# Kernel tuning notes

Measured on AMD Instinct MI355X. Metric: run time of the kernel, lower is better.

The kernel has to match this reference:

```python
import jax, jax.numpy as jnp
import numpy as np

B, S, D = 16, 2048, 128


def setup_inputs() -> dict:
    k = jax.random.key(0)
    k1, k2, k3, k4 = jax.random.split(k, 4)
    query = jax.random.normal(k1, (B, S, D), dtype=jnp.float32)
    key = jax.random.normal(k2, (B, S, D), dtype=jnp.float32)
    value = jax.random.normal(k3, (B, S, D), dtype=jnp.float32)
    # per-query tensor-valued inverse scale; shift away from zero for stable division
    inv_scale_factor = jax.random.uniform(k4, (B, S, 1), dtype=jnp.float32) + 0.5
    dropout_p = jnp.float32(0.1)
    return {"query": query, "key": key, "value": value,
            "inv_scale_factor": inv_scale_factor, "dropout_p": dropout_p}


def reference(query, key, value, inv_scale_factor, dropout_p):
    # QK^T: [B, Sq, Sk]
    qk = jnp.einsum('bqd,bkd->bqk', query, key)
    # tensor-valued scale divide (broadcast [B, Sq, 1] over keys)
    scaled_qk = qk / inv_scale_factor
    softmax_qk = jax.nn.softmax(scaled_qk, axis=-1)
    # dropout with a fixed RNG key (deterministic reference)
    keep_prob = 1.0 - dropout_p
    mask = jax.random.bernoulli(jax.random.key(42), keep_prob, softmax_qk.shape)
    dropout_qk = jnp.where(mask, softmax_qk / keep_prob, jnp.float32(0.0))
    # AV: [B, Sq, Dv]
    return jnp.einsum('bqk,bkv->bqv', dropout_qk, value)
```

## Files before the change

kernel.cpp:

```cpp
#include <hip/hip_runtime.h>
#include <stdint.h>


#define B_ 16
#define S_ 2048
#define D_ 128
#define TQ 64
#define TK 64
#define KSTR 136
#define VSTR 72
#define PSTR 40

typedef float f32x4 __attribute__((ext_vector_type(4)));
typedef _Float16 f16x8 __attribute__((ext_vector_type(8)));
typedef _Float16 f16x2 __attribute__((ext_vector_type(2)));

#define DPP_ROR(x, ctrl) \
  __int_as_float(__builtin_amdgcn_update_dpp(0, __float_as_int(x), (ctrl), 0xf, 0xf, true))
__device__ __forceinline__ float row16_max(float x) {
  x = fmaxf(x, DPP_ROR(x, 0x128));
  x = fmaxf(x, DPP_ROR(x, 0x124));
  x = fmaxf(x, DPP_ROR(x, 0x122));
  x = fmaxf(x, DPP_ROR(x, 0x121));
  return x;
}
__device__ __forceinline__ float row16_sum(float x) {
  x += DPP_ROR(x, 0x128);
  x += DPP_ROR(x, 0x124);
  x += DPP_ROR(x, 0x122);
  x += DPP_ROR(x, 0x121);
  return x;
}

__device__ __forceinline__ uint2 threefry2x32_0_42(uint32_t x0, uint32_t x1) {
  const uint32_t k0 = 0u, k1 = 42u;
  const uint32_t k2 = 0x1BD11BDAu ^ k0 ^ k1;
  x0 += k0; x1 += k1;
#define TFR(r) { x0 += x1; x1 = __builtin_rotateleft32(x1, r); x1 ^= x0; }
  TFR(13) TFR(15) TFR(26) TFR(6)
  x0 += k1; x1 += k2 + 1u;
  TFR(17) TFR(29) TFR(16) TFR(24)
  x0 += k2; x1 += k0 + 2u;
  TFR(13) TFR(15) TFR(26) TFR(6)
  x0 += k0; x1 += k1 + 3u;
  TFR(17) TFR(29) TFR(16) TFR(24)
  x0 += k1; x1 += k2 + 4u;
  TFR(13) TFR(15) TFR(26) TFR(6)
  x0 += k2; x1 += k0 + 5u;
#undef TFR
  return make_uint2(x0, x1);
}

__device__ __forceinline__ uint32_t jax_bits(uint32_t j) {
  const uint2 tf = threefry2x32_0_42(0u, j);
  return tf.x ^ tf.y;
}

__global__ __launch_bounds__(512, 4)
void attn_mfma_kernel(const float* __restrict__ Q, const float* __restrict__ K,
                      const float* __restrict__ V, const float* __restrict__ ISF,
                      const float* __restrict__ DP, float* __restrict__ OUT) {
  __shared__ __align__(16) char smem[46080];
  _Float16* const sK  = (_Float16*)smem;
  _Float16* const sVT = (_Float16*)(smem + 17408);
  _Float16* const sP  = (_Float16*)(smem + 35840);
  float* const sO1 = (float*)smem;
  float* const sM1 = (float*)(smem + 32768);
  float* const sL1 = (float*)(smem + 33024);

  const int t    = threadIdx.x;
  const int lane = t & 63;
  const int l15  = lane & 15;
  const int quad = lane >> 4;
  const int w    = t >> 6;
  const int qg   = w & 3;
  const int kph  = w >> 2;
  const int b    = blockIdx.y;
  const int qw   = blockIdx.x * TQ + qg * 16;

  const float kp = 1.0f - DP[0];
  const uint32_t TH9 = (__float_as_uint(1.0f + kp) & 0x7FFFFFu) << 9;

  float m_[4], l_[4];
  uint32_t jq[4];
  #pragma unroll
  for (int r = 0; r < 4; ++r) {
    m_[r] = -INFINITY;
    l_[r] = 0.0f;
    jq[r] = ((uint32_t)b << 22) + (uint32_t)(qw + quad * 4 + r) * (uint32_t)S_;
  }

  f16x8 qf[4];
  {
    const float qs = 1.4426950408889634f / ISF[b * S_ + qw + l15];
    const float* qp = Q + ((size_t)(b * S_ + qw + l15)) * D_;
    #pragma unroll
    for (int c = 0; c < 4; ++c) {
      const float4 a = *(const float4*)(qp + c * 32 + quad * 8);
      const float4 d2 = *(const float4*)(qp + c * 32 + quad * 8 + 4);
      const float xs[8] = {a.x, a.y, a.z, a.w, d2.x, d2.y, d2.z, d2.w};
      f16x8 h;
      #pragma unroll
      for (int j = 0; j < 8; ++j) h[j] = (_Float16)(xs[j] * qs);
      qf[c] = h;
    }
  }

  f32x4 accO[8];
  #pragma unroll
  for (int i = 0; i < 8; ++i) accO[i] = (f32x4){0.f, 0.f, 0.f, 0.f};

  _Float16* const pwv = &sP[w * 16 * PSTR];

  const int krow = t >> 3, kcol = (t & 7) * 16;
  const int vp = t & 31, dseg = (t >> 5) * 8;

  for (int kt = 0; kt < S_ / TK; ++kt) {
    __syncthreads();

    {
      const float* gk = K + ((size_t)(b * S_ + kt * TK + krow)) * D_ + kcol;
      float kf[16];
      #pragma unroll
      for (int i = 0; i < 4; ++i) *(float4*)&kf[i * 4] = *(const float4*)(gk + i * 4);
      #pragma unroll
      for (int g = 0; g < 2; ++g) {
        f16x8 h;
        #pragma unroll
        for (int j = 0; j < 8; ++j) h[j] = (_Float16)kf[g * 8 + j];
        *(f16x8*)&sK[krow * KSTR + kcol + g * 8] = h;
      }
    }
    {
      const float* gv = V + ((size_t)(b * S_ + kt * TK + 2 * vp)) * D_ + dseg;
      float v0[8], v1[8];
      #pragma unroll
      for (int i = 0; i < 2; ++i) {
        *(float4*)&v0[i * 4] = *(const float4*)(gv + i * 4);
        *(float4*)&v1[i * 4] = *(const float4*)(gv + D_ + i * 4);
      }
      #pragma unroll
      for (int d = 0; d < 8; ++d) {
        f16x2 h = {(_Float16)v0[d], (_Float16)v1[d]};
        *(f16x2*)&sVT[(dseg + d) * VSTR + 2 * vp] = h;
      }
    }
    __syncthreads();

    f32x4 s[2];
    #pragma unroll
    for (int n = 0; n < 2; ++n) {
      f32x4 acc = (f32x4){0.f, 0.f, 0.f, 0.f};
      #pragma unroll
      for (int c = 0; c < 4; ++c) {
        const f16x8 bh = *(const f16x8*)&sK[(kph * 32 + n * 16 + l15) * KSTR + c * 32 + quad * 8];
        acc = __builtin_amdgcn_mfma_f32_16x16x32_f16(qf[c], bh, acc, 0, 0, 0);
      }
      s[n] = acc;
    }

    float mx[4];
    #pragma unroll
    for (int r = 0; r < 4; ++r) mx[r] = row16_max(fmaxf(s[0][r], s[1][r]));
    int changed = 0;
    #pragma unroll
    for (int r = 0; r < 4; ++r) changed |= (mx[r] > m_[r]);
    if (__ballot(changed) != 0ull) {
      #pragma unroll
      for (int r = 0; r < 4; ++r) {
        const float mnew = fmaxf(m_[r], mx[r]);
        const float alpha = __builtin_amdgcn_exp2f(m_[r] - mnew);
        m_[r] = mnew;
        l_[r] *= alpha;
        #pragma unroll
        for (int i = 0; i < 8; ++i) accO[i][r] *= alpha;
      }
    }
    #pragma unroll
    for (int r = 0; r < 4; ++r) {
      const float p0 = __builtin_amdgcn_exp2f(s[0][r] - m_[r]);
      const float p1 = __builtin_amdgcn_exp2f(s[1][r] - m_[r]);
      s[0][r] = p0; s[1][r] = p1;
      l_[r] += row16_sum(p0 + p1);
    }

    #pragma unroll
    for (int n = 0; n < 2; ++n) {
      const int col = n * 16 + l15;
      const uint32_t jcol = (uint32_t)(kt * TK + kph * 32 + col);
      #pragma unroll
      for (int r = 0; r < 4; ++r) {
        const uint32_t bits = jax_bits(jq[r] + jcol);
        const float pf = (bits < TH9) ? s[n][r] : 0.0f;
        pwv[(quad * 4 + r) * PSTR + col] = (_Float16)pf;
      }
    }
    __threadfence_block();

    {
      const f16x8 ap = *(const f16x8*)&pwv[l15 * PSTR + quad * 8];
      #pragma unroll
      for (int d8 = 0; d8 < 8; ++d8) {
        const f16x8 bv = *(const f16x8*)&sVT[(d8 * 16 + l15) * VSTR + kph * 32 + quad * 8];
        accO[d8] = __builtin_amdgcn_mfma_f32_16x16x32_f16(ap, bv, accO[d8], 0, 0, 0);
      }
    }
  }

  __syncthreads();
  if (kph == 1) {
    if (l15 == 0) {
      #pragma unroll
      for (int r = 0; r < 4; ++r) {
        sM1[qg * 16 + quad * 4 + r] = m_[r];
        sL1[qg * 16 + quad * 4 + r] = l_[r];
      }
    }
    #pragma unroll
    for (int d8 = 0; d8 < 8; ++d8) {
      #pragma unroll
      for (int r = 0; r < 4; ++r)
        sO1[qg * 2048 + (quad * 4 + r) * D_ + d8 * 16 + l15] = accO[d8][r];
    }
  }
  __syncthreads();
  if (kph == 0) {
    float a0s[4], a1s[4];
    #pragma unroll
    for (int r = 0; r < 4; ++r) {
      const float m1  = sM1[qg * 16 + quad * 4 + r];
      const float l1v = sL1[qg * 16 + quad * 4 + r];
      const float mf = fmaxf(m_[r], m1);
      const float a0 = __builtin_amdgcn_exp2f(m_[r] - mf);
      const float a1 = __builtin_amdgcn_exp2f(m1 - mf);
      const float inv = 1.0f / ((a0 * l_[r] + a1 * l1v) * kp);
      a0s[r] = a0 * inv;
      a1s[r] = a1 * inv;
    }
    float* op = OUT + ((size_t)(b * S_ + qw)) * D_;
    #pragma unroll
    for (int d8 = 0; d8 < 8; ++d8) {
      #pragma unroll
      for (int r = 0; r < 4; ++r) {
        const float o1 = sO1[qg * 2048 + (quad * 4 + r) * D_ + d8 * 16 + l15];
        op[(quad * 4 + r) * D_ + d8 * 16 + l15] = accO[d8][r] * a0s[r] + o1 * a1s[r];
      }
    }
  }
}

extern "C" void kernel_launch(void* const* d_in, const int* in_sizes, int n_in,
                              void* d_out, int out_size, void* d_ws, size_t ws_size,
                              hipStream_t stream) {
  const float* q   = (const float*)d_in[0];
  const float* k   = (const float*)d_in[1];
  const float* v   = (const float*)d_in[2];
  const float* isf = (const float*)d_in[3];
  const float* dp  = (const float*)d_in[4];
  float* out = (float*)d_out;

  dim3 grid(S_ / TQ, B_);
  attn_mfma_kernel<<<grid, dim3(512), 0, stream>>>(q, k, v, isf, dp, out);
}
```

Before: 338.1 us.

## Double query tile per warp and register-prefetch next K/V tile

Each warp now handles 32 query rows (two 16-row sub-tiles) instead of 16. Each K/V tile loaded from global memory, converted to fp16 and staged in shared memory is therefore reused across twice as many queries, and the K fragments read from shared memory feed two MFMAs. The next tile's K/V global loads are issued into registers right after the barrier, so their latency overlaps the current tile's compute. The trade-off is higher register pressure (launch bounds drop to 2 blocks per CU), half as many blocks in the grid (lower occupancy), and 66.5 KB of dynamic shared memory.

```diff
diff --git a/kernel.cpp b/kernel.cpp
--- a/kernel.cpp
+++ b/kernel.cpp
@@ -5,7 +5,7 @@
 #define B_ 16
 #define S_ 2048
 #define D_ 128
-#define TQ 64
+#define TQ 128
 #define TK 64
 #define KSTR 136
 #define VSTR 72
@@ -14,6 +14,8 @@
 typedef float f32x4 __attribute__((ext_vector_type(4)));
 typedef _Float16 f16x8 __attribute__((ext_vector_type(8)));
 typedef _Float16 f16x2 __attribute__((ext_vector_type(2)));
+
+union F32R { float4 q[4]; float f[16]; };
 
 #define DPP_ROR(x, ctrl) \
   __int_as_float(__builtin_amdgcn_update_dpp(0, __float_as_int(x), (ctrl), 0xf, 0xf, true))
@@ -56,17 +58,17 @@
   return tf.x ^ tf.y;
 }
 
-__global__ __launch_bounds__(512, 4)
+__global__ __launch_bounds__(512, 2)
 void attn_mfma_kernel(const float* __restrict__ Q, const float* __restrict__ K,
                       const float* __restrict__ V, const float* __restrict__ ISF,
                       const float* __restrict__ DP, float* __restrict__ OUT) {
-  __shared__ __align__(16) char smem[46080];
+  extern __shared__ __align__(16) char smem[];
   _Float16* const sK  = (_Float16*)smem;
   _Float16* const sVT = (_Float16*)(smem + 17408);
   _Float16* const sP  = (_Float16*)(smem + 35840);
   float* const sO1 = (float*)smem;
-  float* const sM1 = (float*)(smem + 32768);
-  float* const sL1 = (float*)(smem + 33024);
+  float* const sM1 = (float*)(smem + 65536);
+  float* const sL1 = (float*)(smem + 66048);
 
   const int t    = threadIdx.x;
   const int lane = t & 63;
@@ -76,175 +78,218 @@
   const int qg   = w & 3;
   const int kph  = w >> 2;
   const int b    = blockIdx.y;
-  const int qw   = blockIdx.x * TQ + qg * 16;
+  const int qb   = blockIdx.x * TQ + qg * 32;
 
   const float kp = 1.0f - DP[0];
   const uint32_t TH9 = (__float_as_uint(1.0f + kp) & 0x7FFFFFu) << 9;
 
-  float m_[4], l_[4];
-  uint32_t jq[4];
+  float m_[2][4], l_[2][4];
+  uint32_t jq[2][4];
   #pragma unroll
-  for (int r = 0; r < 4; ++r) {
-    m_[r] = -INFINITY;
-    l_[r] = 0.0f;
-    jq[r] = ((uint32_t)b << 22) + (uint32_t)(qw + quad * 4 + r) * (uint32_t)S_;
-  }
-
-  f16x8 qf[4];
-  {
-    const float qs = 1.4426950408889634f / ISF[b * S_ + qw + l15];
-    const float* qp = Q + ((size_t)(b * S_ + qw + l15)) * D_;
+  for (int sub = 0; sub < 2; ++sub)
+    #pragma unroll
+    for (int r = 0; r < 4; ++r) {
+      m_[sub][r] = -INFINITY;
+      l_[sub][r] = 0.0f;
+      jq[sub][r] = ((uint32_t)b << 22)
+                 + (uint32_t)(qb + sub * 16 + quad * 4 + r) * (uint32_t)S_;
+    }
+
+  f16x8 qf[2][4];
+  #pragma unroll
+  for (int sub = 0; sub < 2; ++sub) {
+    const int qrow = qb + sub * 16 + l15;
+    const float qs = 1.4426950408889634f / ISF[b * S_ + qrow];
+    const float* qp = Q + ((size_t)(b * S_ + qrow)) * D_;
     #pragma unroll
     for (int c = 0; c < 4; ++c) {
-      const float4 a = *(const float4*)(qp + c * 32 + quad * 8);
+      const float4 a  = *(const float4*)(qp + c * 32 + quad * 8);
       const float4 d2 = *(const float4*)(qp + c * 32 + quad * 8 + 4);
       const float xs[8] = {a.x, a.y, a.z, a.w, d2.x, d2.y, d2.z, d2.w};
       f16x8 h;
       #pragma unroll
       for (int j = 0; j < 8; ++j) h[j] = (_Float16)(xs[j] * qs);
-      qf[c] = h;
-    }
-  }
-
-  f32x4 accO[8];
+      qf[sub][c] = h;
+    }
+  }
+
+  f32x4 accO[2][8];
   #pragma unroll
-  for (int i = 0; i < 8; ++i) accO[i] = (f32x4){0.f, 0.f, 0.f, 0.f};
-
-  _Float16* const pwv = &sP[w * 16 * PSTR];
+  for (int sub = 0; sub < 2; ++sub)
+    #pragma unroll
+    for (int i = 0; i < 8; ++i) accO[sub][i] = (f32x4){0.f, 0.f, 0.f, 0.f};
+
+  _Float16* const pwv = &sP[w * 32 * PSTR];
 
   const int krow = t >> 3, kcol = (t & 7) * 16;
   const int vp = t & 31, dseg = (t >> 5) * 8;
 
+  F32R kreg;
+  F32R vreg;
+
+#define ISSUE_LOADS(KT)                                                        \
+  {                                                                            \
+    const float4* gk4 = (const float4*)(K +                                    \
+        ((size_t)(b * S_ + (KT) * TK + krow)) * D_ + kcol);                    \
+    _Pragma("unroll") for (int i = 0; i < 4; ++i) kreg.q[i] = gk4[i];          \
+    const float4* gv4 = (const float4*)(V +                                    \
+        ((size_t)(b * S_ + (KT) * TK + 2 * vp)) * D_ + dseg);                  \
+    _Pragma("unroll") for (int i = 0; i < 2; ++i) {                            \
+      vreg.q[i] = gv4[i];                                                      \
+      vreg.q[i + 2] = gv4[i + 32];             \
+    }                                                                          \
+  }
+
+  ISSUE_LOADS(0)
+
   for (int kt = 0; kt < S_ / TK; ++kt) {
     __syncthreads();
 
     {
-      const float* gk = K + ((size_t)(b * S_ + kt * TK + krow)) * D_ + kcol;
-      float kf[16];
-      #pragma unroll
-      for (int i = 0; i < 4; ++i) *(float4*)&kf[i * 4] = *(const float4*)(gk + i * 4);
       #pragma unroll
       for (int g = 0; g < 2; ++g) {
         f16x8 h;
         #pragma unroll
-        for (int j = 0; j < 8; ++j) h[j] = (_Float16)kf[g * 8 + j];
+        for (int j = 0; j < 8; ++j) h[j] = (_Float16)kreg.f[g * 8 + j];
         *(f16x8*)&sK[krow * KSTR + kcol + g * 8] = h;
       }
     }
     {
-      const float* gv = V + ((size_t)(b * S_ + kt * TK + 2 * vp)) * D_ + dseg;
-      float v0[8], v1[8];
-      #pragma unroll
-      for (int i = 0; i < 2; ++i) {
-        *(float4*)&v0[i * 4] = *(const float4*)(gv + i * 4);
-        *(float4*)&v1[i * 4] = *(const float4*)(gv + D_ + i * 4);
-      }
       #pragma unroll
       for (int d = 0; d < 8; ++d) {
-        f16x2 h = {(_Float16)v0[d], (_Float16)v1[d]};
+        f16x2 h = {(_Float16)vreg.f[d], (_Float16)vreg.f[8 + d]};
         *(f16x2*)&sVT[(dseg + d) * VSTR + 2 * vp] = h;
       }
     }
     __syncthreads();
 
-    f32x4 s[2];
+    if (kt + 1 < S_ / TK) ISSUE_LOADS(kt + 1)
+
+    f32x4 s[2][2];
     #pragma unroll
     for (int n = 0; n < 2; ++n) {
-      f32x4 acc = (f32x4){0.f, 0.f, 0.f, 0.f};
+      f32x4 a0 = (f32x4){0.f, 0.f, 0.f, 0.f};
+      f32x4 a1 = (f32x4){0.f, 0.f, 0.f, 0.f};
       #pragma unroll
       for (int c = 0; c < 4; ++c) {
-        const f16x8 bh = *(const f16x8*)&sK[(kph * 32 + n * 16 + l15) * KSTR + c * 32 + quad * 8];
-        acc = __builtin_amdgcn_mfma_f32_16x16x32_f16(qf[c], bh, acc, 0, 0, 0);
-      }
-      s[n] = acc;
-    }
-
-    float mx[4];
-    #pragma unroll
-    for (int r = 0; r < 4; ++r) mx[r] = row16_max(fmaxf(s[0][r], s[1][r]));
+        const f16x8 bh = *(const f16x8*)&sK[(kph * 32 + n * 16 + l15) * KSTR
+                                            + c * 32 + quad * 8];
+        a0 = __builtin_amdgcn_mfma_f32_16x16x32_f16(qf[0][c], bh, a0, 0, 0, 0);
+        a1 = __builtin_amdgcn_mfma_f32_16x16x32_f16(qf[1][c], bh, a1, 0, 0, 0);
+      }
+      s[0][n] = a0;
+      s[1][n] = a1;
+    }
+
+    float mx[2][4];
     int changed = 0;
     #pragma unroll
-    for (int r = 0; r < 4; ++r) changed |= (mx[r] > m_[r]);
+    for (int sub = 0; sub < 2; ++sub)
+      #pragma unroll
+      for (int r = 0; r < 4; ++r) {
+        mx[sub][r] = row16_max(fmaxf(s[sub][0][r], s[sub][1][r]));
+        changed |= (mx[sub][r] > m_[sub][r]);
+      }
     if (__ballot(changed) != 0ull) {
       #pragma unroll
+      for (int sub = 0; sub < 2; ++sub)
+        #pragma unroll
+        for (int r = 0; r < 4; ++r) {
+          const float mnew = fmaxf(m_[sub][r], mx[sub][r]);
+          const float alpha = __builtin_amdgcn_exp2f(m_[sub][r] - mnew);
+          m_[sub][r] = mnew;
+          l_[sub][r] *= alpha;
+          #pragma unroll
+          for (int i = 0; i < 8; ++i) accO[sub][i][r] *= alpha;
+        }
+    }
+    #pragma unroll
+    for (int sub = 0; sub < 2; ++sub)
+      #pragma unroll
       for (int r = 0; r < 4; ++r) {
-        const float mnew = fmaxf(m_[r], mx[r]);
-        const float alpha = __builtin_amdgcn_exp2f(m_[r] - mnew);
-        m_[r] = mnew;
-        l_[r] *= alpha;
-        #pragma unroll
-        for (int i = 0; i < 8; ++i) accO[i][r] *= alpha;
-      }
-    }
-    #pragma unroll
-    for (int r = 0; r < 4; ++r) {
-      const float p0 = __builtin_amdgcn_exp2f(s[0][r] - m_[r]);
-      const float p1 = __builtin_amdgcn_exp2f(s[1][r] - m_[r]);
-      s[0][r] = p0; s[1][r] = p1;
-      l_[r] += row16_sum(p0 + p1);
-    }
-
-    #pragma unroll
-    for (int n = 0; n < 2; ++n) {
-      const int col = n * 16 + l15;
-      const uint32_t jcol = (uint32_t)(kt * TK + kph * 32 + col);
-      #pragma unroll
-      for (int r = 0; r < 4; ++r) {
-        const uint32_t bits = jax_bits(jq[r] + jcol);
-        const float pf = (bits < TH9) ? s[n][r] : 0.0f;
-        pwv[(quad * 4 + r) * PSTR + col] = (_Float16)pf;
-      }
-    }
+        const float p0 = __builtin_amdgcn_exp2f(s[sub][0][r] - m_[sub][r]);
+        const float p1 = __builtin_amdgcn_exp2f(s[sub][1][r] - m_[sub][r]);
+        s[sub][0][r] = p0;
+        s[sub][1][r] = p1;
+        l_[sub][r] += row16_sum(p0 + p1);
+      }
+
+    #pragma unroll
+    for (int sub = 0; sub < 2; ++sub)
+      #pragma unroll
+      for (int n = 0; n < 2; ++n) {
+        const int col = n * 16 + l15;
+        const uint32_t jcol = (uint32_t)(kt * TK + kph * 32 + col);
+        #pragma unroll
+        for (int r = 0; r < 4; ++r) {
+          const uint32_t bits = jax_bits(jq[sub][r] + jcol);
+          const float pf = (bits < TH9) ? s[sub][n][r] : 0.0f;
+          pwv[(sub * 16 + quad * 4 + r) * PSTR + col] = (_Float16)pf;
+        }
+      }
     __threadfence_block();
 
     {
-      const f16x8 ap = *(const f16x8*)&pwv[l15 * PSTR + quad * 8];
+      const f16x8 ap0 = *(const f16x8*)&pwv[l15 * PSTR + quad * 8];
+      const f16x8 ap1 = *(const f16x8*)&pwv[(16 + l15) * PSTR + quad * 8];
       #pragma unroll
       for (int d8 = 0; d8 < 8; ++d8) {
-        const f16x8 bv = *(const f16x8*)&sVT[(d8 * 16 + l15) * VSTR + kph * 32 + quad * 8];
-        accO[d8] = __builtin_amdgcn_mfma_f32_16x16x32_f16(ap, bv, accO[d8], 0, 0, 0);
-      }
-    }
-  }
+        const f16x8 bv = *(const f16x8*)&sVT[(d8 * 16 + l15) * VSTR
+                                             + kph * 32 + quad * 8];
+        accO[0][d8] = __builtin_amdgcn_mfma_f32_16x16x32_f16(ap0, bv, accO[0][d8], 0, 0, 0);
+        accO[1][d8] = __builtin_amdgcn_mfma_f32_16x16x32_f16(ap1, bv, accO[1][d8], 0, 0, 0);
+      }
+    }
+  }
+#undef ISSUE_LOADS
 
   __syncthreads();
   if (kph == 1) {
-    if (l15 == 0) {
-      #pragma unroll
-      for (int r = 0; r < 4; ++r) {
-        sM1[qg * 16 + quad * 4 + r] = m_[r];
-        sL1[qg * 16 + quad * 4 + r] = l_[r];
-      }
-    }
-    #pragma unroll
-    for (int d8 = 0; d8 < 8; ++d8) {
-      #pragma unroll
-      for (int r = 0; r < 4; ++r)
-        sO1[qg * 2048 + (quad * 4 + r) * D_ + d8 * 16 + l15] = accO[d8][r];
+    #pragma unroll
+    for (int sub = 0; sub < 2; ++sub) {
+      if (l15 == 0) {
+        #pragma unroll
+        for (int r = 0; r < 4; ++r) {
+          const int gr = qg * 32 + sub * 16 + quad * 4 + r;
+          sM1[gr] = m_[sub][r];
+          sL1[gr] = l_[sub][r];
+        }
+      }
+      #pragma unroll
+      for (int d8 = 0; d8 < 8; ++d8)
+        #pragma unroll
+        for (int r = 0; r < 4; ++r) {
+          const int gr = qg * 32 + sub * 16 + quad * 4 + r;
+          sO1[gr * D_ + d8 * 16 + l15] = accO[sub][d8][r];
+        }
     }
   }
   __syncthreads();
   if (kph == 0) {
-    float a0s[4], a1s[4];
-    #pragma unroll
-    for (int r = 0; r < 4; ++r) {
-      const float m1  = sM1[qg * 16 + quad * 4 + r];
-      const float l1v = sL1[qg * 16 + quad * 4 + r];
-      const float mf = fmaxf(m_[r], m1);
-      const float a0 = __builtin_amdgcn_exp2f(m_[r] - mf);
-      const float a1 = __builtin_amdgcn_exp2f(m1 - mf);
-      const float inv = 1.0f / ((a0 * l_[r] + a1 * l1v) * kp);
-      a0s[r] = a0 * inv;
-      a1s[r] = a1 * inv;
-    }
-    float* op = OUT + ((size_t)(b * S_ + qw)) * D_;
-    #pragma unroll
-    for (int d8 = 0; d8 < 8; ++d8) {
+    #pragma unroll
+    for (int sub = 0; sub < 2; ++sub) {
+      float a0s[4], a1s[4];
       #pragma unroll
       for (int r = 0; r < 4; ++r) {
-        const float o1 = sO1[qg * 2048 + (quad * 4 + r) * D_ + d8 * 16 + l15];
-        op[(quad * 4 + r) * D_ + d8 * 16 + l15] = accO[d8][r] * a0s[r] + o1 * a1s[r];
-      }
+        const int gr = qg * 32 + sub * 16 + quad * 4 + r;
+        const float m1  = sM1[gr];
+        const float l1v = sL1[gr];
+        const float mf = fmaxf(m_[sub][r], m1);
+        const float a0 = __builtin_amdgcn_exp2f(m_[sub][r] - mf);
+        const float a1 = __builtin_amdgcn_exp2f(m1 - mf);
+        const float inv = 1.0f / ((a0 * l_[sub][r] + a1 * l1v) * kp);
+        a0s[r] = a0 * inv;
+        a1s[r] = a1 * inv;
+      }
+      #pragma unroll
+      for (int d8 = 0; d8 < 8; ++d8)
+        #pragma unroll
+        for (int r = 0; r < 4; ++r) {
+          const int gr = qg * 32 + sub * 16 + quad * 4 + r;
+          const float o1 = sO1[gr * D_ + d8 * 16 + l15];
+          OUT[((size_t)(b * S_ + blockIdx.x * TQ + gr)) * D_ + d8 * 16 + l15] =
+              accO[sub][d8][r] * a0s[r] + o1 * a1s[r];
+        }
     }
   }
 }
@@ -260,5 +305,5 @@
   float* out = (float*)d_out;
 
   dim3 grid(S_ / TQ, B_);
-  attn_mfma_kernel<<<grid, dim3(512), 0, stream>>>(q, k, v, isf, dp, out);
-}
+  attn_mfma_kernel<<<grid, dim3(512), 66560, stream>>>(q, k, v, isf, dp, out);
+}
```

Measured after the change: 288.1 us. 1.17x faster.

## Double-buffer K/V tiles with register prefetch and double the query tile

Applied to the files above, without the earlier changes.

Doubles the query tile per block to 128 rows with 1024 threads, so each K/V tile staged in LDS is reused by twice as many query rows. The kernel now double-buffers K and V^T in LDS, using 92 KB of dynamic shared memory, and prefetches the next tile into registers while the current one is being computed. That removes one barrier per iteration and hides global-load latency. The dropout RNG bits are computed right after QK^T so the hash overlaps the softmax reductions. In exchange the grid shrinks to 256 blocks, which lowers parallelism, and the larger LDS footprint and register pressure may limit occupancy or cause spills.

```diff
diff --git a/kernel.cpp b/kernel.cpp
--- a/kernel.cpp
+++ b/kernel.cpp
@@ -5,8 +5,9 @@
 #define B_ 16
 #define S_ 2048
 #define D_ 128
-#define TQ 64
+#define TQ 128
 #define TK 64
+#define NT (S_ / TK)
 #define KSTR 136
 #define VSTR 72
 #define PSTR 40
@@ -14,6 +15,8 @@
 typedef float f32x4 __attribute__((ext_vector_type(4)));
 typedef _Float16 f16x8 __attribute__((ext_vector_type(8)));
 typedef _Float16 f16x2 __attribute__((ext_vector_type(2)));
+
+union F32R { float4 q[2]; float f[8]; };
 
 #define DPP_ROR(x, ctrl) \
   __int_as_float(__builtin_amdgcn_update_dpp(0, __float_as_int(x), (ctrl), 0xf, 0xf, true))
@@ -56,27 +59,29 @@
   return tf.x ^ tf.y;
 }
 
-__global__ __launch_bounds__(512, 4)
+__global__ __launch_bounds__(1024, 4)
 void attn_mfma_kernel(const float* __restrict__ Q, const float* __restrict__ K,
                       const float* __restrict__ V, const float* __restrict__ ISF,
                       const float* __restrict__ DP, float* __restrict__ OUT) {
-  __shared__ __align__(16) char smem[46080];
-  _Float16* const sK  = (_Float16*)smem;
-  _Float16* const sVT = (_Float16*)(smem + 17408);
-  _Float16* const sP  = (_Float16*)(smem + 35840);
+  extern __shared__ __align__(16) char smem[];
+  _Float16* const sK0  = (_Float16*)smem;
+  _Float16* const sK1  = (_Float16*)(smem + 17408);
+  _Float16* const sVT0 = (_Float16*)(smem + 34816);
+  _Float16* const sVT1 = (_Float16*)(smem + 53248);
+  _Float16* const sP   = (_Float16*)(smem + 71680);
   float* const sO1 = (float*)smem;
-  float* const sM1 = (float*)(smem + 32768);
-  float* const sL1 = (float*)(smem + 33024);
+  float* const sM1 = (float*)(smem + 65536);
+  float* const sL1 = (float*)(smem + 66048);
 
   const int t    = threadIdx.x;
   const int lane = t & 63;
   const int l15  = lane & 15;
   const int quad = lane >> 4;
   const int w    = t >> 6;
-  const int qg   = w & 3;
-  const int kph  = w >> 2;
+  const int qg   = w & 7;
+  const int kph  = w >> 3;
   const int b    = blockIdx.y;
-  const int qw   = blockIdx.x * TQ + qg * 16;
+  const int qb   = blockIdx.x * TQ + qg * 16;
 
   const float kp = 1.0f - DP[0];
   const uint32_t TH9 = (__float_as_uint(1.0f + kp) & 0x7FFFFFu) << 9;
@@ -87,16 +92,18 @@
   for (int r = 0; r < 4; ++r) {
     m_[r] = -INFINITY;
     l_[r] = 0.0f;
-    jq[r] = ((uint32_t)b << 22) + (uint32_t)(qw + quad * 4 + r) * (uint32_t)S_;
+    jq[r] = ((uint32_t)b << 22)
+          + (uint32_t)(qb + quad * 4 + r) * (uint32_t)S_;
   }
 
   f16x8 qf[4];
   {
-    const float qs = 1.4426950408889634f / ISF[b * S_ + qw + l15];
-    const float* qp = Q + ((size_t)(b * S_ + qw + l15)) * D_;
+    const int qrow = qb + l15;
+    const float qs = 1.4426950408889634f / ISF[b * S_ + qrow];
+    const float* qp = Q + ((size_t)(b * S_ + qrow)) * D_;
     #pragma unroll
     for (int c = 0; c < 4; ++c) {
-      const float4 a = *(const float4*)(qp + c * 32 + quad * 8);
+      const float4 a  = *(const float4*)(qp + c * 32 + quad * 8);
       const float4 d2 = *(const float4*)(qp + c * 32 + quad * 8 + 4);
       const float xs[8] = {a.x, a.y, a.z, a.w, d2.x, d2.y, d2.z, d2.w};
       f16x8 h;
@@ -112,40 +119,45 @@
 
   _Float16* const pwv = &sP[w * 16 * PSTR];
 
-  const int krow = t >> 3, kcol = (t & 7) * 16;
-  const int vp = t & 31, dseg = (t >> 5) * 8;
-
-  for (int kt = 0; kt < S_ / TK; ++kt) {
-    __syncthreads();
-
-    {
-      const float* gk = K + ((size_t)(b * S_ + kt * TK + krow)) * D_ + kcol;
-      float kf[16];
-      #pragma unroll
-      for (int i = 0; i < 4; ++i) *(float4*)&kf[i * 4] = *(const float4*)(gk + i * 4);
-      #pragma unroll
-      for (int g = 0; g < 2; ++g) {
-        f16x8 h;
-        #pragma unroll
-        for (int j = 0; j < 8; ++j) h[j] = (_Float16)kf[g * 8 + j];
-        *(f16x8*)&sK[krow * KSTR + kcol + g * 8] = h;
-      }
-    }
-    {
-      const float* gv = V + ((size_t)(b * S_ + kt * TK + 2 * vp)) * D_ + dseg;
-      float v0[8], v1[8];
-      #pragma unroll
-      for (int i = 0; i < 2; ++i) {
-        *(float4*)&v0[i * 4] = *(const float4*)(gv + i * 4);
-        *(float4*)&v1[i * 4] = *(const float4*)(gv + D_ + i * 4);
-      }
-      #pragma unroll
-      for (int d = 0; d < 8; ++d) {
-        f16x2 h = {(_Float16)v0[d], (_Float16)v1[d]};
-        *(f16x2*)&sVT[(dseg + d) * VSTR + 2 * vp] = h;
-      }
-    }
-    __syncthreads();
+  const int krow = t >> 4, kcol = (t & 15) * 8;
+  const int vp = t & 31, dseg = (t >> 5) * 4;
+
+  F32R kreg;
+  F32R vreg;
+
+#define ISSUE_LOADS(KT)                                                        \
+  {                                                                            \
+    const float4* gk4 = (const float4*)(K +                                    \
+        ((size_t)(b * S_ + (KT) * TK + krow)) * D_ + kcol);                    \
+    kreg.q[0] = gk4[0];                                                        \
+    kreg.q[1] = gk4[1];                                                        \
+    const float4* gv4 = (const float4*)(V +                                    \
+        ((size_t)(b * S_ + (KT) * TK + 2 * vp)) * D_ + dseg);                  \
+    vreg.q[0] = gv4[0];                                                        \
+    vreg.q[1] = gv4[32];                       \
+  }
+
+#define CONVERT_TO(KB, VB)                                                     \
+  {                                                                            \
+    f16x8 h;                                                                   \
+    _Pragma("unroll") for (int j = 0; j < 8; ++j)                              \
+      h[j] = (_Float16)kreg.f[j];                                              \
+    *(f16x8*)&(KB)[krow * KSTR + kcol] = h;                                    \
+    _Pragma("unroll") for (int d = 0; d < 4; ++d) {                            \
+      f16x2 h2 = {(_Float16)vreg.f[d], (_Float16)vreg.f[4 + d]};               \
+      *(f16x2*)&(VB)[(dseg + d) * VSTR + 2 * vp] = h2;                         \
+    }                                                                          \
+  }
+
+  ISSUE_LOADS(0)
+  CONVERT_TO(sK0, sVT0)
+  ISSUE_LOADS(1)
+  __syncthreads();
+
+  for (int kt = 0; kt < NT; ++kt) {
+    const int cur = kt & 1;
+    _Float16* const sKc = cur ? sK1 : sK0;
+    _Float16* const sVc = cur ? sVT1 : sVT0;
 
     f32x4 s[2];
     #pragma unroll
@@ -153,18 +165,29 @@
       f32x4 acc = (f32x4){0.f, 0.f, 0.f, 0.f};
       #pragma unroll
       for (int c = 0; c < 4; ++c) {
-        const f16x8 bh = *(const f16x8*)&sK[(kph * 32 + n * 16 + l15) * KSTR + c * 32 + quad * 8];
+        const f16x8 bh = *(const f16x8*)&sKc[(kph * 32 + n * 16 + l15) * KSTR
+                                             + c * 32 + quad * 8];
         acc = __builtin_amdgcn_mfma_f32_16x16x32_f16(qf[c], bh, acc, 0, 0, 0);
       }
       s[n] = acc;
     }
 
+    uint32_t rb[2][4];
+    #pragma unroll
+    for (int n = 0; n < 2; ++n) {
+      const uint32_t jcol = (uint32_t)(kt * TK + kph * 32 + n * 16 + l15);
+      #pragma unroll
+      for (int r = 0; r < 4; ++r)
+        rb[n][r] = jax_bits(jq[r] + jcol);
+    }
+
     float mx[4];
-    #pragma unroll
-    for (int r = 0; r < 4; ++r) mx[r] = row16_max(fmaxf(s[0][r], s[1][r]));
     int changed = 0;
     #pragma unroll
-    for (int r = 0; r < 4; ++r) changed |= (mx[r] > m_[r]);
+    for (int r = 0; r < 4; ++r) {
+      mx[r] = row16_max(fmaxf(s[0][r], s[1][r]));
+      changed |= (mx[r] > m_[r]);
+    }
     if (__ballot(changed) != 0ull) {
       #pragma unroll
       for (int r = 0; r < 4; ++r) {
@@ -180,18 +203,17 @@
     for (int r = 0; r < 4; ++r) {
       const float p0 = __builtin_amdgcn_exp2f(s[0][r] - m_[r]);
       const float p1 = __builtin_amdgcn_exp2f(s[1][r] - m_[r]);
-      s[0][r] = p0; s[1][r] = p1;
+      s[0][r] = p0;
+      s[1][r] = p1;
       l_[r] += row16_sum(p0 + p1);
     }
 
     #pragma unroll
     for (int n = 0; n < 2; ++n) {
       const int col = n * 16 + l15;
-      const uint32_t jcol = (uint32_t)(kt * TK + kph * 32 + col);
-      #pragma unroll
-      for (int r = 0; r < 4; ++r) {
-        const uint32_t bits = jax_bits(jq[r] + jcol);
-        const float pf = (bits < TH9) ? s[n][r] : 0.0f;
+      #pragma unroll
+      for (int r = 0; r < 4; ++r) {
+        const float pf = (rb[n][r] < TH9) ? s[n][r] : 0.0f;
         pwv[(quad * 4 + r) * PSTR + col] = (_Float16)pf;
       }
     }
@@ -201,35 +223,48 @@
       const f16x8 ap = *(const f16x8*)&pwv[l15 * PSTR + quad * 8];
       #pragma unroll
       for (int d8 = 0; d8 < 8; ++d8) {
-        const f16x8 bv = *(const f16x8*)&sVT[(d8 * 16 + l15) * VSTR + kph * 32 + quad * 8];
+        const f16x8 bv = *(const f16x8*)&sVc[(d8 * 16 + l15) * VSTR
+                                             + kph * 32 + quad * 8];
         accO[d8] = __builtin_amdgcn_mfma_f32_16x16x32_f16(ap, bv, accO[d8], 0, 0, 0);
       }
     }
-  }
-
-  __syncthreads();
+
+    if (kt + 1 < NT) {
+      _Float16* const sKn = cur ? sK0 : sK1;
+      _Float16* const sVn = cur ? sVT0 : sVT1;
+      CONVERT_TO(sKn, sVn)
+      if (kt + 2 < NT) ISSUE_LOADS(kt + 2)
+    }
+    __syncthreads();
+  }
+#undef ISSUE_LOADS
+#undef CONVERT_TO
+
   if (kph == 1) {
     if (l15 == 0) {
       #pragma unroll
       for (int r = 0; r < 4; ++r) {
-        sM1[qg * 16 + quad * 4 + r] = m_[r];
-        sL1[qg * 16 + quad * 4 + r] = l_[r];
-      }
-    }
-    #pragma unroll
-    for (int d8 = 0; d8 < 8; ++d8) {
-      #pragma unroll
-      for (int r = 0; r < 4; ++r)
-        sO1[qg * 2048 + (quad * 4 + r) * D_ + d8 * 16 + l15] = accO[d8][r];
-    }
+        const int gr = qg * 16 + quad * 4 + r;
+        sM1[gr] = m_[r];
+        sL1[gr] = l_[r];
+      }
+    }
+    #pragma unroll
+    for (int d8 = 0; d8 < 8; ++d8)
+      #pragma unroll
+      for (int r = 0; r < 4; ++r) {
+        const int gr = qg * 16 + quad * 4 + r;
+        sO1[gr * D_ + d8 * 16 + l15] = accO[d8][r];
+      }
   }
   __syncthreads();
   if (kph == 0) {
     float a0s[4], a1s[4];
     #pragma unroll
     for (int r = 0; r < 4; ++r) {
-      const float m1  = sM1[qg * 16 + quad * 4 + r];
-      const float l1v = sL1[qg * 16 + quad * 4 + r];
+      const int gr = qg * 16 + quad * 4 + r;
+      const float m1  = sM1[gr];
+      const float l1v = sL1[gr];
       const float mf = fmaxf(m_[r], m1);
       const float a0 = __builtin_amdgcn_exp2f(m_[r] - mf);
       const float a1 = __builtin_amdgcn_exp2f(m1 - mf);
@@ -237,15 +272,15 @@
       a0s[r] = a0 * inv;
       a1s[r] = a1 * inv;
     }
-    float* op = OUT + ((size_t)(b * S_ + qw)) * D_;
-    #pragma unroll
-    for (int d8 = 0; d8 < 8; ++d8) {
-      #pragma unroll
-      for (int r = 0; r < 4; ++r) {
-        const float o1 = sO1[qg * 2048 + (quad * 4 + r) * D_ + d8 * 16 + l15];
-        op[(quad * 4 + r) * D_ + d8 * 16 + l15] = accO[d8][r] * a0s[r] + o1 * a1s[r];
-      }
-    }
+    #pragma unroll
+    for (int d8 = 0; d8 < 8; ++d8)
+      #pragma unroll
+      for (int r = 0; r < 4; ++r) {
+        const int gr = qg * 16 + quad * 4 + r;
+        const float o1 = sO1[gr * D_ + d8 * 16 + l15];
+        OUT[((size_t)(b * S_ + blockIdx.x * TQ + gr)) * D_ + d8 * 16 + l15] =
+            accO[d8][r] * a0s[r] + o1 * a1s[r];
+      }
   }
 }
 
@@ -260,5 +295,5 @@
   float* out = (float*)d_out;
 
   dim3 grid(S_ / TQ, B_);
-  attn_mfma_kernel<<<grid, dim3(512), 0, stream>>>(q, k, v, isf, dp, out);
-}
+  attn_mfma_kernel<<<grid, dim3(1024), 92160, stream>>>(q, k, v, isf, dp, out);
+}
```

After: 308.0 us. 8.9% less time.
